# Kernel optimization log

Hardware: AMD Instinct MI355X
Metric: run time of the kernel (lower is better)

## Reference

```python
import jax, jax.numpy as jnp
import numpy as np

# Physical parameters (match init_kwargs['params'])
P = dict(A_he=1.0, alpha_he=10.0, c_p=4186.0, c_p_sw=4000.0, rho=1000.0, rho_sw=1025.0,
         A_sf=500.0, beta=0.5, H=4.0, L_a=10.0, n_cs=10, c1=60000.0, TV=10.0, UA1=100.0, UA2=100.0)

T_STEPS, BATCH = 4096, 2048


def setup_inputs() -> dict:
    key = jax.random.key(0)
    ks = jax.random.split(key, 6)
    sh = (T_STEPS, BATCH)
    u = lambda k: jax.random.uniform(k, sh, dtype=jnp.float32)
    return {
        'V_sequence': 0.3 * u(ks[0]),             # mixing valve fraction in [0, 0.3)
        'I_sequence': 200.0 + 800.0 * u(ks[1]),   # solar irradiance W/m^2
        'T_a_sequence': 15.0 + 15.0 * u(ks[2]),   # ambient temperature C
        'F1_sequence': 50.0 + 100.0 * u(ks[3]),   # solar-field flow L/min
        'F2_sequence': 20.0 + 20.0 * u(ks[4]),    # hot-side HE flow L/min
        'F3_sequence': 100.0 + 50.0 * u(ks[5]),   # seawater flow L/min
        'dt': 60,
        'simulation_time': T_STEPS * 60,
    }


def _simulate(V, I, Ta, F1, F2, F3, dtf):
    rho, c_p, c_p_sw, rho_sw = P['rho'], P['c_p'], P['c_p_sw'], P['rho_sw']
    A_sf, beta, H, c1 = P['A_sf'], P['beta'], P['H'], P['c1']
    L_eq = P['L_a'] * P['n_cs']
    TV, UA1, UA2 = P['TV'], P['UA1'], P['UA2']
    aA = P['alpha_he'] * P['A_he']
    B_ = V.shape[1]
    f = lambda v: jnp.full((B_,), v, dtype=jnp.float32)
    # initial states: T1, T2, T3, T4, T6, T8
    init = (f(50.0), f(60.0), f(60.0), f(50.0), f(25.0), f(60.0))

    def step(carry, xs):
        T1, T2, T3, T4, T6, T8 = carry
        V_t, I_t, Ta_t, F1_t, F2_t, F3_t = xs
        # --- solar field (explicit Euler) ---
        m_1 = F1_t * rho / c1
        T_avg = (T1 + T2) * 0.5
        dT2 = (beta * I_t - H / L_eq * (T_avg - Ta_t)
               - c_p * m_1 * (T2 - T1) / L_eq) / (A_sf * rho * c_p)
        T2n = T2 + dT2 * dtf
        # --- mass flows ---
        m1z = F1_t * rho / 60000.0
        m2 = (1.0 - V_t) * F2_t * rho / 60000.0
        m3 = F2_t * rho / 60000.0
        m4 = F3_t * rho_sw / 60000.0
        # --- storage tank two-node model (both derivatives use old T3, T4) ---
        dT3 = (m1z * T2n + m2 * T4 - m1z * T3 - m2 * T3 - UA1 * (T3 - Ta_t) / c_p) / (rho * TV)
        dT4 = (m1z * T3 + m2 * T6 - m1z * T4 - m2 * T4 - UA2 * (T4 - Ta_t) / c_p) / (rho * TV)
        T3n = T3 + dT3 * dtf
        T4n = T4 + dT4 * dtf
        T1n = T4n
        # --- mixing + heat exchanger ---
        T5 = V_t * T6 + (1.0 - V_t) * T3n
        T7 = T8 - 4.0
        theta = aA * (1.0 / (m3 * c_p) - 1.0 / (m4 * c_p_sw))
        e = jnp.exp(theta)
        Ahe = 1.0 - e
        Bhe = m3 * c_p / (m4 * c_p_sw) * e
        eta1 = Ahe / (1.1 - Bhe)
        eta2 = m3 * c_p / (m4 * c_p_sw)
        T6n = T5 - 1.6 * eta1 * (T5 - T7)
        T8n = T7 + 0.45 * eta2 * (T5 - T6n)
        return (T1n, T2n, T3n, T4n, T6n, T8n), (T2n, T3n, T4n, T5, T6n, T7, T8n)

    _, hist = jax.lax.scan(step, init, (V, I, Ta, F1, F2, F3))
    # stacked histories: [7, T, B] in order (T2, T3, T4, T5, T6, T7, T8)
    return jnp.stack(hist, axis=0)


def reference(V_sequence, I_sequence, T_a_sequence, F1_sequence, F2_sequence, F3_sequence, dt, simulation_time):
    steps = simulation_time // dt  # == T_STEPS here
    sl = lambda x: x[:steps]
    return _simulate(sl(V_sequence), sl(I_sequence), sl(T_a_sequence),
                     sl(F1_sequence), sl(F2_sequence), sl(F3_sequence), float(dt))
```

## Files before the change

### kernel.cpp

```cpp
#include <hip/hip_runtime.h>


#define T_STEPS 4096
#define BATCH   2048
#define NCHUNK  128
#define CLEN    32

typedef float f2 __attribute__((ext_vector_type(2)));

struct StepScal {
    float v, ta, m1, m2, m12, cpLm1, e16, e245, cst2, kq, rdt;
};

__device__ __forceinline__ float exp_small(float x)
{
    if (__builtin_expect(fabsf(x) < 0.008f, 1)) {
        float x2 = x * x;
        return 1.0f + x + x2 * 0.5f + x2 * x * (1.0f / 6.0f);
    }
    return expf(x);
}

__device__ __forceinline__ StepScal make_scal(
    float v, float ii, float ta, float f1, float f2_, float f3,
    float kq, float rdt)
{
    StepScal sc;
    sc.v  = v;
    sc.ta = ta;
    sc.m1 = f1 * (1.0f/60.0f);
    sc.m2 = (1.0f - v) * f2_ * (1.0f/60.0f);
    sc.m12 = sc.m1 + sc.m2;
    sc.cpLm1 = 41.86f * sc.m1;
    float a_ = f2_ * (4186.0f/60.0f);
    float b_ = f3 * (1025.0f*4000.0f/60000.0f);
    float ra = 1.0f / a_;
    float rb = 1.0f / b_;
    float rc = a_ * rb;
    float theta = 10.0f * (ra - rb);
    float e = exp_small(theta);
    float eta1 = (1.0f - e) / (1.1f - rc * e);
    sc.e16  = 1.6f  * eta1;
    sc.e245 = 0.45f * rc;
    sc.cst2 = 0.5f * ii + 0.04f * ta;
    sc.kq = kq;
    sc.rdt = rdt;
    return sc;
}

template<bool OFF, bool EMIT>
__device__ __forceinline__ void smd_step(float s[5], const StepScal& sc, float* o)
{
    const float UA_CP = 100.0f / 4186.0f;
    float t2 = s[0], t3 = s[1], t4 = s[2], t6 = s[3], t8 = s[4];

    float lin = -0.04f * (0.5f * (t4 + t2)) - sc.cpLm1 * (t2 - t4);
    if (OFF) lin += sc.cst2;
    float t2n = t2 + sc.kq * lin;

    float x3 = OFF ? (t3 - sc.ta) : t3;
    float x4 = OFF ? (t4 - sc.ta) : t4;
    float c3 = sc.m1 * t2n + sc.m2 * t4 - sc.m12 * t3 - UA_CP * x3;
    float c4 = sc.m1 * t3  + sc.m2 * t6 - sc.m12 * t4 - UA_CP * x4;
    float t3n = t3 + sc.rdt * c3;
    float t4n = t4 + sc.rdt * c4;

    float t5 = sc.v * t6 + (1.0f - sc.v) * t3n;
    float t7 = OFF ? (t8 - 4.0f) : t8;
    float t6n = t5 - sc.e16 * (t5 - t7);
    float t8n = t7 + sc.e245 * (t5 - t6n);

    s[0] = t2n; s[1] = t3n; s[2] = t4n; s[3] = t6n; s[4] = t8n;
    if (EMIT) {
        o[0] = t2n; o[1] = t3n; o[2] = t4n; o[3] = t5;
        o[4] = t6n; o[5] = t7;  o[6] = t8n;
    }
}

__global__ __launch_bounds__(256, 4) void phaseA(
    const float* __restrict__ V, const float* __restrict__ I,
    const float* __restrict__ Ta, const float* __restrict__ F1,
    const float* __restrict__ F2, const float* __restrict__ F3,
    const int* __restrict__ dtp, float* __restrict__ maps)
{
    const int b = blockIdx.x * blockDim.x + threadIdx.x;
    const int c = blockIdx.y;
    const float dtf = (float)dtp[0];
    const float kq  = dtf * (1.0f / 2.093e9f);
    const float rdt = dtf * 1e-4f;

    float s[6][5];
#pragma unroll
    for (int j = 0; j < 6; ++j)
#pragma unroll
        for (int i = 0; i < 5; ++i) s[j][i] = (i == j) ? 1.0f : 0.0f;

    int idx = c * CLEN * BATCH + b;
#pragma unroll 2
    for (int k = 0; k < CLEN; ++k, idx += BATCH) {
        StepScal sc = make_scal(V[idx], I[idx], Ta[idx], F1[idx], F2[idx], F3[idx], kq, rdt);
#pragma unroll
        for (int j = 0; j < 5; ++j) smd_step<false, false>(s[j], sc, nullptr);
        smd_step<true, false>(s[5], sc, nullptr);
    }

    float tmp[32];
#pragma unroll
    for (int j = 0; j < 6; ++j)
#pragma unroll
        for (int i = 0; i < 5; ++i) tmp[j * 5 + i] = s[j][i];
    tmp[30] = 0.0f; tmp[31] = 0.0f;
    float4* mp = (float4*)(maps + ((size_t)b * NCHUNK + c) * 32);
#pragma unroll
    for (int k = 0; k < 8; ++k) mp[k] = ((const float4*)tmp)[k];
}

__global__ void phaseB(const float* __restrict__ maps,
                       float* __restrict__ states)
{
    __shared__ float lds[NCHUNK * 33];
    const int b = blockIdx.x;
    const int c = threadIdx.x;

    float tmp[32];
    const float4* mp = (const float4*)(maps + ((size_t)b * NCHUNK + c) * 32);
#pragma unroll
    for (int k = 0; k < 8; ++k) ((float4*)tmp)[k] = mp[k];
    float m[30];
#pragma unroll
    for (int k = 0; k < 30; ++k) m[k] = tmp[k];

#pragma unroll
    for (int d = 1; d < NCHUNK; d <<= 1) {
#pragma unroll
        for (int k = 0; k < 30; ++k) lds[c * 33 + k] = m[k];
        __syncthreads();
        float o[30];
        const bool act = (c >= d);
        if (act) {
#pragma unroll
            for (int k = 0; k < 30; ++k) o[k] = lds[(c - d) * 33 + k];
        }
        __syncthreads();
        if (act) {
            float nm[30];
#pragma unroll
            for (int j = 0; j < 5; ++j)
#pragma unroll
                for (int i = 0; i < 5; ++i) {
                    float acc = m[0 * 5 + i] * o[j * 5 + 0];
#pragma unroll
                    for (int k = 1; k < 5; ++k)
                        acc = fmaf(m[k * 5 + i], o[j * 5 + k], acc);
                    nm[j * 5 + i] = acc;
                }
#pragma unroll
            for (int i = 0; i < 5; ++i) {
                float acc = m[25 + i];
#pragma unroll
                for (int k = 0; k < 5; ++k)
                    acc = fmaf(m[k * 5 + i], o[25 + k], acc);
                nm[25 + i] = acc;
            }
#pragma unroll
            for (int k = 0; k < 30; ++k) m[k] = nm[k];
        }
    }

#pragma unroll
    for (int k = 0; k < 30; ++k) lds[c * 33 + k] = m[k];
    __syncthreads();

    const float s0[5] = {60.0f, 60.0f, 50.0f, 25.0f, 60.0f};
    float st[8];
#pragma unroll
    for (int i = 0; i < 5; ++i) st[i] = s0[i];
    st[5] = 0.0f; st[6] = 0.0f; st[7] = 0.0f;
    if (c > 0) {
        const float* pm = &lds[(c - 1) * 33];
#pragma unroll
        for (int i = 0; i < 5; ++i) {
            float acc = pm[25 + i];
#pragma unroll
            for (int j = 0; j < 5; ++j)
                acc = fmaf(pm[j * 5 + i], s0[j], acc);
            st[i] = acc;
        }
    }
    float4* op = (float4*)(states + ((size_t)c * BATCH + b) * 8);
    op[0] = ((const float4*)st)[0];
    op[1] = ((const float4*)st)[1];
}

__global__ __launch_bounds__(256, 4) void phaseC(
    const float* __restrict__ V, const float* __restrict__ I,
    const float* __restrict__ Ta, const float* __restrict__ F1,
    const float* __restrict__ F2, const float* __restrict__ F3,
    const int* __restrict__ dtp, const float* __restrict__ states,
    float* __restrict__ out)
{
    const int pair = blockIdx.x * blockDim.x + threadIdx.x;
    const int b = pair * 2;
    const int c = blockIdx.y;
    const float dtf = (float)dtp[0];
    const float kq  = dtf * (1.0f / 2.093e9f);
    const float rdt = dtf * 1e-4f;

    const float* sp = states + ((size_t)c * BATCH + b) * 8;
    float s0v[5], s1v[5];
#pragma unroll
    for (int i = 0; i < 5; ++i) { s0v[i] = sp[i]; s1v[i] = sp[8 + i]; }

    int idx = c * CLEN * BATCH + b;
#pragma unroll 4
    for (int k = 0; k < CLEN; ++k, idx += BATCH) {
        f2 v2  = *(const f2*)&V[idx];
        f2 i2  = *(const f2*)&I[idx];
        f2 ta2 = *(const f2*)&Ta[idx];
        f2 f12 = *(const f2*)&F1[idx];
        f2 f22 = *(const f2*)&F2[idx];
        f2 f32 = *(const f2*)&F3[idx];
        StepScal sca = make_scal(v2.x, i2.x, ta2.x, f12.x, f22.x, f32.x, kq, rdt);
        StepScal scb = make_scal(v2.y, i2.y, ta2.y, f12.y, f22.y, f32.y, kq, rdt);
        float oa[7], ob[7];
        smd_step<true, true>(s0v, sca, oa);
        smd_step<true, true>(s1v, scb, ob);
#pragma unroll
        for (int q = 0; q < 7; ++q) {
            f2 w; w.x = oa[q]; w.y = ob[q];
            __builtin_nontemporal_store(w, (f2*)&out[q * (T_STEPS * BATCH) + idx]);
        }
    }
}

__global__ __launch_bounds__(256) void serialK(
    const float* __restrict__ V, const float* __restrict__ I,
    const float* __restrict__ Ta, const float* __restrict__ F1,
    const float* __restrict__ F2, const float* __restrict__ F3,
    const int* __restrict__ dtp, float* __restrict__ out)
{
    const int b = blockIdx.x * blockDim.x + threadIdx.x;
    const float dtf = (float)dtp[0];
    const float kq  = dtf * (1.0f / 2.093e9f);
    const float rdt = dtf * 1e-4f;
    float s[5] = {60.0f, 60.0f, 50.0f, 25.0f, 60.0f};
    int idx = b;
    for (int t = 0; t < T_STEPS; ++t, idx += BATCH) {
        StepScal sc = make_scal(V[idx], I[idx], Ta[idx], F1[idx], F2[idx], F3[idx], kq, rdt);
        float o[7];
        smd_step<true, true>(s, sc, o);
#pragma unroll
        for (int q = 0; q < 7; ++q)
            __builtin_nontemporal_store(o[q], &out[q * (T_STEPS * BATCH) + idx]);
    }
}

extern "C" void kernel_launch(void* const* d_in, const int* in_sizes, int n_in,
                              void* d_out, int out_size, void* d_ws, size_t ws_size,
                              hipStream_t stream)
{
    const float* V  = (const float*)d_in[0];
    const float* I  = (const float*)d_in[1];
    const float* Ta = (const float*)d_in[2];
    const float* F1 = (const float*)d_in[3];
    const float* F2 = (const float*)d_in[4];
    const float* F3 = (const float*)d_in[5];
    const int*  dtp = (const int*)d_in[6];
    float* out = (float*)d_out;

    const size_t need = ((size_t)NCHUNK * BATCH * 32 + (size_t)NCHUNK * BATCH * 8) * sizeof(float);
    if (need <= ws_size) {
        float* maps   = (float*)d_ws;
        float* states = maps + (size_t)BATCH * NCHUNK * 32;
        hipLaunchKernelGGL(phaseA, dim3(BATCH / 256, NCHUNK), dim3(256), 0, stream,
                           V, I, Ta, F1, F2, F3, dtp, maps);
        hipLaunchKernelGGL(phaseB, dim3(BATCH), dim3(NCHUNK), 0, stream,
                           maps, states);
        hipLaunchKernelGGL(phaseC, dim3(BATCH / 512, NCHUNK), dim3(256), 0, stream,
                           V, I, Ta, F1, F2, F3, dtp, states, out);
    } else {
        hipLaunchKernelGGL(serialK, dim3(BATCH / 256), dim3(256), 0, stream,
                           V, I, Ta, F1, F2, F3, dtp, out);
    }
}
```

Baseline: 150.9 us.

## Process two batch lanes per thread in phaseA and add nontemporal workspace traffic

phaseA now handles two adjacent batch columns per thread with float2 input loads, halving its grid and doubling per-thread register state (two 6x5 affine maps). Workspace stores and loads in all phases become nontemporal vector accesses, and launch bounds drop to 3 waves per SIMD for A and C. make_scal replaces two reciprocals with one reciprocal of a product. The register pressure of 60 live map entries may cause spills or lower occupancy, and the reciprocal rewrite slightly changes rounding.

After: 216.7 us. 1.44x slower.

```diff
diff --git a/kernel.cpp b/kernel.cpp
--- a/kernel.cpp
+++ b/kernel.cpp
@@ -7,6 +7,7 @@
 #define CLEN    32
 
 typedef float f2 __attribute__((ext_vector_type(2)));
+typedef float f4 __attribute__((ext_vector_type(4)));
 
 struct StepScal {
     float v, ta, m1, m2, m12, cpLm1, e16, e245, cst2, kq, rdt;
@@ -34,10 +35,9 @@
     sc.cpLm1 = 41.86f * sc.m1;
     float a_ = f2_ * (4186.0f/60.0f);
     float b_ = f3 * (1025.0f*4000.0f/60000.0f);
-    float ra = 1.0f / a_;
-    float rb = 1.0f / b_;
-    float rc = a_ * rb;
-    float theta = 10.0f * (ra - rb);
+    float inv_ab = 1.0f / (a_ * b_);
+    float rc    = a_ * a_ * inv_ab;
+    float theta = 10.0f * (b_ - a_) * inv_ab;
     float e = exp_small(theta);
     float eta1 = (1.0f - e) / (1.1f - rc * e);
     sc.e16  = 1.6f  * eta1;
@@ -77,127 +77,11 @@
     }
 }
 
-__global__ __launch_bounds__(256, 4) void phaseA(
+__global__ __launch_bounds__(256, 3) void phaseA(
     const float* __restrict__ V, const float* __restrict__ I,
     const float* __restrict__ Ta, const float* __restrict__ F1,
     const float* __restrict__ F2, const float* __restrict__ F3,
     const int* __restrict__ dtp, float* __restrict__ maps)
-{
-    const int b = blockIdx.x * blockDim.x + threadIdx.x;
-    const int c = blockIdx.y;
-    const float dtf = (float)dtp[0];
-    const float kq  = dtf * (1.0f / 2.093e9f);
-    const float rdt = dtf * 1e-4f;
-
-    float s[6][5];
-#pragma unroll
-    for (int j = 0; j < 6; ++j)
-#pragma unroll
-        for (int i = 0; i < 5; ++i) s[j][i] = (i == j) ? 1.0f : 0.0f;
-
-    int idx = c * CLEN * BATCH + b;
-#pragma unroll 2
-    for (int k = 0; k < CLEN; ++k, idx += BATCH) {
-        StepScal sc = make_scal(V[idx], I[idx], Ta[idx], F1[idx], F2[idx], F3[idx], kq, rdt);
-#pragma unroll
-        for (int j = 0; j < 5; ++j) smd_step<false, false>(s[j], sc, nullptr);
-        smd_step<true, false>(s[5], sc, nullptr);
-    }
-
-    float tmp[32];
-#pragma unroll
-    for (int j = 0; j < 6; ++j)
-#pragma unroll
-        for (int i = 0; i < 5; ++i) tmp[j * 5 + i] = s[j][i];
-    tmp[30] = 0.0f; tmp[31] = 0.0f;
-    float4* mp = (float4*)(maps + ((size_t)b * NCHUNK + c) * 32);
-#pragma unroll
-    for (int k = 0; k < 8; ++k) mp[k] = ((const float4*)tmp)[k];
-}
-
-__global__ void phaseB(const float* __restrict__ maps,
-                       float* __restrict__ states)
-{
-    __shared__ float lds[NCHUNK * 33];
-    const int b = blockIdx.x;
-    const int c = threadIdx.x;
-
-    float tmp[32];
-    const float4* mp = (const float4*)(maps + ((size_t)b * NCHUNK + c) * 32);
-#pragma unroll
-    for (int k = 0; k < 8; ++k) ((float4*)tmp)[k] = mp[k];
-    float m[30];
-#pragma unroll
-    for (int k = 0; k < 30; ++k) m[k] = tmp[k];
-
-#pragma unroll
-    for (int d = 1; d < NCHUNK; d <<= 1) {
-#pragma unroll
-        for (int k = 0; k < 30; ++k) lds[c * 33 + k] = m[k];
-        __syncthreads();
-        float o[30];
-        const bool act = (c >= d);
-        if (act) {
-#pragma unroll
-            for (int k = 0; k < 30; ++k) o[k] = lds[(c - d) * 33 + k];
-        }
-        __syncthreads();
-        if (act) {
-            float nm[30];
-#pragma unroll
-            for (int j = 0; j < 5; ++j)
-#pragma unroll
-                for (int i = 0; i < 5; ++i) {
-                    float acc = m[0 * 5 + i] * o[j * 5 + 0];
-#pragma unroll
-                    for (int k = 1; k < 5; ++k)
-                        acc = fmaf(m[k * 5 + i], o[j * 5 + k], acc);
-                    nm[j * 5 + i] = acc;
-                }
-#pragma unroll
-            for (int i = 0; i < 5; ++i) {
-                float acc = m[25 + i];
-#pragma unroll
-                for (int k = 0; k < 5; ++k)
-                    acc = fmaf(m[k * 5 + i], o[25 + k], acc);
-                nm[25 + i] = acc;
-            }
-#pragma unroll
-            for (int k = 0; k < 30; ++k) m[k] = nm[k];
-        }
-    }
-
-#pragma unroll
-    for (int k = 0; k < 30; ++k) lds[c * 33 + k] = m[k];
-    __syncthreads();
-
-    const float s0[5] = {60.0f, 60.0f, 50.0f, 25.0f, 60.0f};
-    float st[8];
-#pragma unroll
-    for (int i = 0; i < 5; ++i) st[i] = s0[i];
-    st[5] = 0.0f; st[6] = 0.0f; st[7] = 0.0f;
-    if (c > 0) {
-        const float* pm = &lds[(c - 1) * 33];
-#pragma unroll
-        for (int i = 0; i < 5; ++i) {
-            float acc = pm[25 + i];
-#pragma unroll
-            for (int j = 0; j < 5; ++j)
-                acc = fmaf(pm[j * 5 + i], s0[j], acc);
-            st[i] = acc;
-        }
-    }
-    float4* op = (float4*)(states + ((size_t)c * BATCH + b) * 8);
-    op[0] = ((const float4*)st)[0];
-    op[1] = ((const float4*)st)[1];
-}
-
-__global__ __launch_bounds__(256, 4) void phaseC(
-    const float* __restrict__ V, const float* __restrict__ I,
-    const float* __restrict__ Ta, const float* __restrict__ F1,
-    const float* __restrict__ F2, const float* __restrict__ F3,
-    const int* __restrict__ dtp, const float* __restrict__ states,
-    float* __restrict__ out)
 {
     const int pair = blockIdx.x * blockDim.x + threadIdx.x;
     const int b = pair * 2;
@@ -206,10 +90,151 @@
     const float kq  = dtf * (1.0f / 2.093e9f);
     const float rdt = dtf * 1e-4f;
 
-    const float* sp = states + ((size_t)c * BATCH + b) * 8;
-    float s0v[5], s1v[5];
-#pragma unroll
-    for (int i = 0; i < 5; ++i) { s0v[i] = sp[i]; s1v[i] = sp[8 + i]; }
+    float sA[6][5], sB[6][5];
+#pragma unroll
+    for (int j = 0; j < 6; ++j)
+#pragma unroll
+        for (int i = 0; i < 5; ++i) {
+            sA[j][i] = (i == j) ? 1.0f : 0.0f;
+            sB[j][i] = (i == j) ? 1.0f : 0.0f;
+        }
+
+    int idx = c * CLEN * BATCH + b;
+#pragma unroll 2
+    for (int k = 0; k < CLEN; ++k, idx += BATCH) {
+        f2 v2  = *(const f2*)&V[idx];
+        f2 i2  = *(const f2*)&I[idx];
+        f2 ta2 = *(const f2*)&Ta[idx];
+        f2 f12 = *(const f2*)&F1[idx];
+        f2 f22 = *(const f2*)&F2[idx];
+        f2 f32 = *(const f2*)&F3[idx];
+        StepScal sca = make_scal(v2.x, i2.x, ta2.x, f12.x, f22.x, f32.x, kq, rdt);
+        StepScal scb = make_scal(v2.y, i2.y, ta2.y, f12.y, f22.y, f32.y, kq, rdt);
+#pragma unroll
+        for (int j = 0; j < 5; ++j) smd_step<false, false>(sA[j], sca, nullptr);
+        smd_step<true, false>(sA[5], sca, nullptr);
+#pragma unroll
+        for (int j = 0; j < 5; ++j) smd_step<false, false>(sB[j], scb, nullptr);
+        smd_step<true, false>(sB[5], scb, nullptr);
+    }
+
+    float tmpA[32], tmpB[32];
+#pragma unroll
+    for (int j = 0; j < 6; ++j)
+#pragma unroll
+        for (int i = 0; i < 5; ++i) {
+            tmpA[j * 5 + i] = sA[j][i];
+            tmpB[j * 5 + i] = sB[j][i];
+        }
+    tmpA[30] = tmpA[31] = tmpB[30] = tmpB[31] = 0.0f;
+    f4* mpA = (f4*)(maps + ((size_t)b * NCHUNK + c) * 32);
+    f4* mpB = (f4*)(maps + ((size_t)(b + 1) * NCHUNK + c) * 32);
+#pragma unroll
+    for (int k = 0; k < 8; ++k) {
+        __builtin_nontemporal_store(((const f4*)tmpA)[k], mpA + k);
+        __builtin_nontemporal_store(((const f4*)tmpB)[k], mpB + k);
+    }
+}
+
+__global__ void phaseB(const float* __restrict__ maps,
+                       float* __restrict__ states)
+{
+    __shared__ float lds[NCHUNK * 33];
+    const int b = blockIdx.x;
+    const int c = threadIdx.x;
+
+    float tmp[32];
+    const f4* mp = (const f4*)(maps + ((size_t)b * NCHUNK + c) * 32);
+#pragma unroll
+    for (int k = 0; k < 8; ++k)
+        ((f4*)tmp)[k] = __builtin_nontemporal_load(mp + k);
+    float m[30];
+#pragma unroll
+    for (int k = 0; k < 30; ++k) m[k] = tmp[k];
+
+#pragma unroll
+    for (int d = 1; d < NCHUNK; d <<= 1) {
+#pragma unroll
+        for (int k = 0; k < 30; ++k) lds[c * 33 + k] = m[k];
+        __syncthreads();
+        float o[30];
+        const bool act = (c >= d);
+        if (act) {
+#pragma unroll
+            for (int k = 0; k < 30; ++k) o[k] = lds[(c - d) * 33 + k];
+        }
+        __syncthreads();
+        if (act) {
+            float nm[30];
+#pragma unroll
+            for (int j = 0; j < 5; ++j)
+#pragma unroll
+                for (int i = 0; i < 5; ++i) {
+                    float acc = m[0 * 5 + i] * o[j * 5 + 0];
+#pragma unroll
+                    for (int k = 1; k < 5; ++k)
+                        acc = fmaf(m[k * 5 + i], o[j * 5 + k], acc);
+                    nm[j * 5 + i] = acc;
+                }
+#pragma unroll
+            for (int i = 0; i < 5; ++i) {
+                float acc = m[25 + i];
+#pragma unroll
+                for (int k = 0; k < 5; ++k)
+                    acc = fmaf(m[k * 5 + i], o[25 + k], acc);
+                nm[25 + i] = acc;
+            }
+#pragma unroll
+            for (int k = 0; k < 30; ++k) m[k] = nm[k];
+        }
+    }
+
+#pragma unroll
+    for (int k = 0; k < 30; ++k) lds[c * 33 + k] = m[k];
+    __syncthreads();
+
+    const float s0[5] = {60.0f, 60.0f, 50.0f, 25.0f, 60.0f};
+    float st[8];
+#pragma unroll
+    for (int i = 0; i < 5; ++i) st[i] = s0[i];
+    st[5] = 0.0f; st[6] = 0.0f; st[7] = 0.0f;
+    if (c > 0) {
+        const float* pm = &lds[(c - 1) * 33];
+#pragma unroll
+        for (int i = 0; i < 5; ++i) {
+            float acc = pm[25 + i];
+#pragma unroll
+            for (int j = 0; j < 5; ++j)
+                acc = fmaf(pm[j * 5 + i], s0[j], acc);
+            st[i] = acc;
+        }
+    }
+    f4* op = (f4*)(states + ((size_t)c * BATCH + b) * 8);
+    __builtin_nontemporal_store(((const f4*)st)[0], op);
+    __builtin_nontemporal_store(((const f4*)st)[1], op + 1);
+}
+
+__global__ __launch_bounds__(256, 3) void phaseC(
+    const float* __restrict__ V, const float* __restrict__ I,
+    const float* __restrict__ Ta, const float* __restrict__ F1,
+    const float* __restrict__ F2, const float* __restrict__ F3,
+    const int* __restrict__ dtp, const float* __restrict__ states,
+    float* __restrict__ out)
+{
+    const int pair = blockIdx.x * blockDim.x + threadIdx.x;
+    const int b = pair * 2;
+    const int c = blockIdx.y;
+    const float dtf = (float)dtp[0];
+    const float kq  = dtf * (1.0f / 2.093e9f);
+    const float rdt = dtf * 1e-4f;
+
+    const f4* sp4 = (const f4*)(states + ((size_t)c * BATCH + b) * 8);
+    f4 q0 = __builtin_nontemporal_load(sp4);
+    f4 q1 = __builtin_nontemporal_load(sp4 + 1);
+    f4 q2 = __builtin_nontemporal_load(sp4 + 2);
+    f4 q3 = __builtin_nontemporal_load(sp4 + 3);
+    float s0v[5] = {q0.x, q0.y, q0.z, q0.w, q1.x};
+    float s1v[5] = {q2.x, q2.y, q2.z, q2.w, q3.x};
 
     int idx = c * CLEN * BATCH + b;
 #pragma unroll 4
@@ -272,7 +297,7 @@
     if (need <= ws_size) {
         float* maps   = (float*)d_ws;
         float* states = maps + (size_t)BATCH * NCHUNK * 32;
-        hipLaunchKernelGGL(phaseA, dim3(BATCH / 256, NCHUNK), dim3(256), 0, stream,
+        hipLaunchKernelGGL(phaseA, dim3(BATCH / 512, NCHUNK), dim3(256), 0, stream,
                            V, I, Ta, F1, F2, F3, dtp, maps);
         hipLaunchKernelGGL(phaseB, dim3(BATCH), dim3(NCHUNK), 0, stream,
                            maps, states);
```
